# Optimization experiments

Measured on AMD Instinct MI355X. Metric: run time of the kernel, lower is better.

## Reference

```python
import jax, jax.numpy as jnp
import numpy as np

N, E = 20000, 320000
D, C = 128, 32          # node_dim, edge_dim
H, QK, V = 12, 32, 32   # heads, query_key_dim, value_dim
QP, VP = 8, 8           # query/value points
EPS_LN = 1e-5


def _lin_init(key, fan_in, fan_out):
    return jax.random.normal(key, (fan_in, fan_out), dtype=jnp.float32) / np.sqrt(fan_in)


def setup_inputs():
    key = jax.random.key(0)
    ks = jax.random.split(key, 24)
    inp = {}
    inp['R'] = jax.random.normal(ks[0], (N, 3, 3), dtype=jnp.float32)
    inp['t'] = jax.random.normal(ks[1], (N, 3), dtype=jnp.float32)
    inp['x'] = jax.random.normal(ks[2], (N, D), dtype=jnp.float32)
    inp['z'] = jax.random.normal(ks[3], (E, C), dtype=jnp.float32)
    inp['edge_index'] = jax.random.randint(ks[4], (2, E), 0, N, dtype=jnp.int64)
    inp['Wq'] = _lin_init(ks[5], D, QK * H)
    inp['Wk'] = _lin_init(ks[6], D, QK * H)
    inp['Wv'] = _lin_init(ks[7], D, V * H)
    inp['Wpair'] = _lin_init(ks[8], C, H)
    inp['spatial_coef'] = jnp.full((1, H), np.log(np.exp(1.0) - 1.0), dtype=jnp.float32)
    inp['Wqp'] = _lin_init(ks[9], D, QP * H * 3)
    inp['Wkp'] = _lin_init(ks[10], D, QP * H * 3)
    inp['Wvp'] = _lin_init(ks[11], D, VP * H * 3)
    d_out_in = H * C + H * V + H * VP * 7  # 384 + 384 + 672 = 1440
    inp['Wo'] = _lin_init(ks[12], d_out_in, D)
    inp['bo'] = jnp.zeros((D,), dtype=jnp.float32)
    inp['ln1_g'] = jnp.ones((D,), dtype=jnp.float32)
    inp['ln1_b'] = jnp.zeros((D,), dtype=jnp.float32)
    inp['mlp_w1'] = _lin_init(ks[13], D, D)
    inp['mlp_b1'] = jnp.zeros((D,), dtype=jnp.float32)
    inp['mlp_w2'] = _lin_init(ks[14], D, D)
    inp['mlp_b2'] = jnp.zeros((D,), dtype=jnp.float32)
    inp['mlp_w3'] = _lin_init(ks[15], D, D)
    inp['mlp_b3'] = jnp.zeros((D,), dtype=jnp.float32)
    inp['ln2_g'] = jnp.ones((D,), dtype=jnp.float32)
    inp['ln2_b'] = jnp.zeros((D,), dtype=jnp.float32)
    return inp


def _scatter_softmax(logits, seg, n):
    # numerically stable per-destination-node softmax over incoming edges
    m = jax.ops.segment_max(logits, seg, num_segments=n)
    m = jnp.where(jnp.isfinite(m), m, 0.0)
    e = jnp.exp(logits - m[seg])
    s = jax.ops.segment_sum(e, seg, num_segments=n)
    return e / s[seg]


def _ln(h, g, b):
    mu = jnp.mean(h, axis=-1, keepdims=True)
    var = jnp.var(h, axis=-1, keepdims=True)
    return (h - mu) / jnp.sqrt(var + EPS_LN) * g + b


def _local_to_global(R, t, p):  # p: (N, P, 3) -> R p + t
    return jnp.einsum('nij,npj->npi', R, p) + t[:, None, :]


def _global_to_local(R, t, q):  # q: (N, P, 3) -> R^T (q - t)
    return jnp.einsum('nji,npj->npi', R, q - t[:, None, :])


def reference(R, t, x, z, edge_index, Wq, Wk, Wv, Wpair, spatial_coef, Wqp, Wkp, Wvp,
              Wo, bo, ln1_g, ln1_b, mlp_w1, mlp_b1, mlp_w2, mlp_b2, mlp_w3, mlp_b3,
              ln2_g, ln2_b):
    n = x.shape[0]
    src, dst = edge_index[0], edge_index[1]

    # --- node logits ---
    q = (x @ Wq).reshape(n, H, QK)
    k = (x @ Wk).reshape(n, H, QK)
    logits_node = jnp.sum(q[src] * k[dst], axis=-1) / np.sqrt(QK)  # (E, H)

    # --- pair logits ---
    logits_pair = z @ Wpair  # (E, H)

    # --- spatial logits ---
    qp = _local_to_global(R, t, (x @ Wqp).reshape(n, H * QP, 3)).reshape(n, H, QP * 3)
    kp = _local_to_global(R, t, (x @ Wkp).reshape(n, H * QP, 3)).reshape(n, H, QP * 3)
    sum_sq_dist = jnp.sum((qp[src] - kp[dst]) ** 2, axis=-1)  # (E, H)
    gamma = jax.nn.softplus(spatial_coef)  # (1, H)
    logits_spatial = sum_sq_dist * (-gamma * np.sqrt(2.0 / (9.0 * QP)) / 2.0)

    logits = (logits_node + logits_pair + logits_spatial) * np.sqrt(1.0 / 3.0)
    alpha = _scatter_softmax(logits, src, n)  # (E, H)

    # --- pair aggregation: (E,H,1)*(E,1,C) scatter-sum -> (N, H*C) ---
    feat_p2n = jax.ops.segment_sum(alpha[:, :, None] * z[:, None, :], src, num_segments=n).reshape(n, -1)

    # --- node aggregation ---
    v = (x @ Wv).reshape(n, H, V)
    feat_node = jax.ops.segment_sum(alpha[:, :, None] * v[dst], src, num_segments=n).reshape(n, -1)

    # --- spatial aggregation ---
    vp = _local_to_global(R, t, (x @ Wvp).reshape(n, H * VP, 3)).reshape(n, H, VP, 3)
    aggr = jax.ops.segment_sum(alpha[:, :, None, None] * vp[dst], src, num_segments=n)  # (N,H,VP,3)
    loc = _global_to_local(R, t, aggr.reshape(n, H * VP, 3))  # (N, H*VP, 3)
    nrm = jnp.linalg.norm(loc, axis=-1)
    dirn = loc / jnp.maximum(nrm[..., None], 1e-8)
    feat_spatial = jnp.concatenate([loc.reshape(n, -1), nrm.reshape(n, -1), dirn.reshape(n, -1)], axis=-1)

    feat_all = jnp.concatenate([feat_p2n, feat_node, feat_spatial], axis=-1) @ Wo + bo
    h = _ln(x + feat_all, ln1_g, ln1_b)
    m = jax.nn.relu(h @ mlp_w1 + mlp_b1)
    m = jax.nn.relu(m @ mlp_w2 + mlp_b2) @ mlp_w3 + mlp_b3
    return _ln(h + m, ln2_g, ln2_b)
```

## Files before the change

### kernel.cpp

```cpp
#include <hip/hip_runtime.h>
#include <hip/hip_bf16.h>
#include <math.h>

#define NN 20000
#define EE 320000
#define PQ_COLS  384
#define PQP_COLS 288
#define PKP_COLS 288
#define QE_COLS  768
#define VE_COLS  672
#define KE_COLS  768
#define FCOLS 1440

typedef __attribute__((ext_vector_type(8))) short bf16x8v;
typedef __attribute__((ext_vector_type(4))) float f32x4v;

__device__ __forceinline__ float b2f(unsigned short u) {
  return __uint_as_float(((unsigned)u) << 16);
}
__device__ __forceinline__ unsigned short f2bu(float f) {
  __hip_bfloat16 h = __float2bfloat16(f);
  return *reinterpret_cast<unsigned short*>(&h);
}

__global__ void cvt_x(const float* __restrict__ x, __hip_bfloat16* __restrict__ XB)
{
  int i = (blockIdx.x*256 + threadIdx.x) * 4;
  if (i >= NN*128) return;
  float4 v = *(const float4*)&x[i];
  XB[i+0] = __float2bfloat16(v.x); XB[i+1] = __float2bfloat16(v.y);
  XB[i+2] = __float2bfloat16(v.z); XB[i+3] = __float2bfloat16(v.w);
}

__global__ void cvt_w(const float* __restrict__ Wq, const float* __restrict__ Wk,
                      const float* __restrict__ Wv, const float* __restrict__ Wqp,
                      const float* __restrict__ Wkp, const float* __restrict__ Wvp,
                      const float* __restrict__ Wo,
                      __hip_bfloat16* __restrict__ WBt, __hip_bfloat16* __restrict__ WoT)
{
  int idx = blockIdx.x*256 + threadIdx.x;
  if (idx < 2016*128) {
    int c = idx >> 7, k = idx & 127;
    float v;
    if      (c < 384)  v = Wq [k*384 + c];
    else if (c < 768)  v = Wk [k*384 + (c-384)];
    else if (c < 1152) v = Wv [k*384 + (c-768)];
    else if (c < 1440) v = Wqp[k*288 + (c-1152)];
    else if (c < 1728) v = Wkp[k*288 + (c-1440)];
    else               v = Wvp[k*288 + (c-1728)];
    WBt[idx] = __float2bfloat16(v);
  } else {
    int j = idx - 2016*128;
    if (j < 128*1440) {
      int c = j / 1440, k = j - c*1440;
      WoT[j] = __float2bfloat16(Wo[k*128 + c]);
    }
  }
}

__global__ __launch_bounds__(256) void proj_mfma(
    const __hip_bfloat16* __restrict__ XB, const __hip_bfloat16* __restrict__ WBt,
    float* __restrict__ Pq, float* __restrict__ Pqp, float* __restrict__ Pkp,
    __hip_bfloat16* __restrict__ KE, __hip_bfloat16* __restrict__ VE)
{
  __shared__ short A_lds[64*136];
  __shared__ short B_lds[128*136];
  const int t = threadIdx.x;
  const int n0 = blockIdx.x * 64;
  const int c0 = blockIdx.y * 128;
  {
    int r = t >> 2, kc = (t & 3) * 32;
    int gr = n0 + r; if (gr >= NN) gr = NN-1;
    const uint4* src = (const uint4*)(XB + (size_t)gr*128 + kc);
    uint4 v0 = src[0], v1 = src[1], v2 = src[2], v3 = src[3];
    *(uint4*)&A_lds[r*136 + kc +  0] = v0;
    *(uint4*)&A_lds[r*136 + kc +  8] = v1;
    *(uint4*)&A_lds[r*136 + kc + 16] = v2;
    *(uint4*)&A_lds[r*136 + kc + 24] = v3;
  }
  {
    int cI = t >> 1, ko = (t & 1) * 64;
    int gc = c0 + cI; if (gc > 2015) gc = 2015;
    const uint4* src = (const uint4*)(WBt + (size_t)gc*128 + ko);
    #pragma unroll
    for (int j = 0; j < 8; j++)
      *(uint4*)&B_lds[cI*136 + ko + j*8] = src[j];
  }
  __syncthreads();
  const int lane = t & 63, wid = t >> 6;
  const int wm = wid >> 1, wn = wid & 1;
  const int lrow = lane >> 4, lcol = lane & 15;
  f32x4v zero = {0.f, 0.f, 0.f, 0.f};
  f32x4v acc[2][4];
  #pragma unroll
  for (int i = 0; i < 2; i++)
    #pragma unroll
    for (int j = 0; j < 4; j++) acc[i][j] = zero;
  #pragma unroll
  for (int ks = 0; ks < 4; ks++) {
    int kb = ks*32 + lrow*8;
    bf16x8v a0 = *(const bf16x8v*)&A_lds[(wm*32 +      lcol)*136 + kb];
    bf16x8v a1 = *(const bf16x8v*)&A_lds[(wm*32 + 16 + lcol)*136 + kb];
    #pragma unroll
    for (int nt = 0; nt < 4; nt++) {
      bf16x8v b = *(const bf16x8v*)&B_lds[(wn*64 + nt*16 + lcol)*136 + kb];
      acc[0][nt] = __builtin_amdgcn_mfma_f32_16x16x32_bf16(a0, b, acc[0][nt], 0, 0, 0);
      acc[1][nt] = __builtin_amdgcn_mfma_f32_16x16x32_bf16(a1, b, acc[1][nt], 0, 0, 0);
    }
  }
  #pragma unroll
  for (int nt = 0; nt < 4; nt++) {
    int colb = c0 + wn*64 + nt*16;
    if (colb >= 2016) continue;
    int col = colb + lcol;
    #pragma unroll
    for (int mt = 0; mt < 2; mt++) {
      #pragma unroll
      for (int r = 0; r < 4; r++) {
        int grow = n0 + wm*32 + mt*16 + lrow*4 + r;
        if (grow >= NN) continue;
        float v = acc[mt][nt][r];
        if      (col < 384)  Pq[(size_t)grow*PQ_COLS + col] = v;
        else if (col < 768)  { int d = col-384; KE[(size_t)grow*KE_COLS + (d>>5)*64 + (d&31)] = __float2bfloat16(v); }
        else if (col < 1152) VE[(size_t)grow*VE_COLS + (col-768)] = __float2bfloat16(v);
        else if (col < 1440) Pqp[(size_t)grow*PQP_COLS + (col-1152)] = v;
        else if (col < 1728) Pkp[(size_t)grow*PKP_COLS + (col-1440)] = v;
        else                 VE[(size_t)grow*VE_COLS + 384 + (col-1728)] = __float2bfloat16(v);
      }
    }
  }
}

__global__ __launch_bounds__(256) void prep_node(
    const float* __restrict__ Pq, const float* __restrict__ Pqp, const float* __restrict__ Pkp,
    const float* __restrict__ R, const float* __restrict__ tr, const float* __restrict__ spc,
    __hip_bfloat16* __restrict__ QE, __hip_bfloat16* __restrict__ KE,
    __hip_bfloat16* __restrict__ VE)
{
  __shared__ float qpg[288];
  __shared__ float skk[12], cf[12];
  const int n = blockIdx.x, t = threadIdx.x;
  if (t < 12) { cf[t] = log1pf(expf(spc[t])) * (1.f/12.f); skk[t] = 0.f; }
  __syncthreads();
  const float* Rn = R + (size_t)n*9;
  const float r0=Rn[0],r1=Rn[1],r2=Rn[2],r3=Rn[3],r4=Rn[4],r5=Rn[5],r6=Rn[6],r7=Rn[7],r8=Rn[8];
  const float t0=tr[n*3],t1=tr[n*3+1],t2=tr[n*3+2];
  for (int task = t; task < 288; task += 256) {
    if (task < 96) {
      const float* p = Pqp + (size_t)n*PQP_COLS + task*3;
      float l0=p[0],l1=p[1],l2=p[2];
      qpg[task*3+0] = r0*l0+r1*l1+r2*l2+t0;
      qpg[task*3+1] = r3*l0+r4*l1+r5*l2+t1;
      qpg[task*3+2] = r6*l0+r7*l1+r8*l2+t2;
    } else if (task < 192) {
      int j = task-96, h = j>>3, jj = j&7;
      const float* p = Pkp + (size_t)n*PKP_COLS + h*24 + jj*3;
      float l0=p[0],l1=p[1],l2=p[2];
      __hip_bfloat16 b0=__float2bfloat16(r0*l0+r1*l1+r2*l2+t0);
      __hip_bfloat16 b1=__float2bfloat16(r3*l0+r4*l1+r5*l2+t1);
      __hip_bfloat16 b2=__float2bfloat16(r6*l0+r7*l1+r8*l2+t2);
      __hip_bfloat16* o = KE + (size_t)n*KE_COLS + h*64 + 32 + jj*3;
      o[0]=b0; o[1]=b1; o[2]=b2;
      float f0=__bfloat162float(b0), f1=__bfloat162float(b1), f2=__bfloat162float(b2);
      atomicAdd(&skk[h], f0*f0 + f1*f1 + f2*f2);
    } else {
      __hip_bfloat16* p = VE + (size_t)n*VE_COLS + 384 + (task-192)*3;
      float l0=__bfloat162float(p[0]), l1=__bfloat162float(p[1]), l2=__bfloat162float(p[2]);
      p[0] = __float2bfloat16(r0*l0+r1*l1+r2*l2+t0);
      p[1] = __float2bfloat16(r3*l0+r4*l1+r5*l2+t1);
      p[2] = __float2bfloat16(r6*l0+r7*l1+r8*l2+t2);
    }
  }
  __syncthreads();
  #pragma unroll
  for (int u = 0; u < 3; u++) {
    int s = t + 256*u;
    int h = s >> 6, i = s & 63;
    float val = 0.f;
    if (i < 32)      val = 0.1020620726f * Pq[(size_t)n*PQ_COLS + h*32 + i];
    else if (i < 56) val = 1.15470053838f * cf[h] * qpg[h*24 + (i-32)];
    else if (i == 58 || i == 59) val = 1.0f;
    QE[(size_t)n*QE_COLS + s] = __float2bfloat16(val);
  }
  if (t < 96) {
    int h = t >> 3, i = t & 7;
    float skkp = -0.57735026919f * cf[h] * skk[h];
    __hip_bfloat16 hi = __float2bfloat16(skkp);
    float res = skkp - __bfloat162float(hi);
    __hip_bfloat16 outv;
    if (i == 2)      outv = hi;
    else if (i == 3) outv = __float2bfloat16(res);
    else             outv = __float2bfloat16(0.0f);
    KE[(size_t)n*KE_COLS + h*64 + 56 + i] = outv;
  }
}

__global__ __launch_bounds__(256) void pl_kernel(
    const float* __restrict__ z, const float* __restrict__ Wpair, float* __restrict__ PL)
{
  __shared__ float wp[384];
  const int t = threadIdx.x;
  for (int i = t; i < 384; i += 256) wp[i] = Wpair[i] * 0.57735026919f;
  __syncthreads();
  int e0 = blockIdx.x * 64;
  #pragma unroll
  for (int u = 0; u < 3; u++) {
    int idx = t + 256*u;
    int q = idx / 12, h = idx - 12*q;
    int e = e0 + q;
    if (q < 64 && e < EE) {
      const float* zr = z + (size_t)e*32;
      float s = 0.f;
      #pragma unroll
      for (int c = 0; c < 32; c++) s += zr[c] * wp[c*12 + h];
      PL[(size_t)e*12 + h] = s;
    }
  }
}

__global__ void count_edges(const int* __restrict__ ei, int* __restrict__ cnt)
{
  int e = blockIdx.x*256 + threadIdx.x;
  if (e < EE) atomicAdd(&cnt[ei[e]], 1);
}

__global__ __launch_bounds__(1024) void scan_csr(const int* __restrict__ cnt,
                                                 int* __restrict__ rowptr,
                                                 int* __restrict__ cursor)
{
  __shared__ int part[1024];
  int t = threadIdx.x;
  int base = t*20;
  int loc[20];
  int s = 0;
  #pragma unroll
  for (int i = 0; i < 20; i++) {
    int idx = base + i;
    int cc = (idx < NN) ? cnt[idx] : 0;
    loc[i] = s; s += cc;
  }
  part[t] = s;
  __syncthreads();
  for (int off = 1; off < 1024; off <<= 1) {
    int v = (t >= off) ? part[t-off] : 0;
    __syncthreads();
    part[t] += v;
    __syncthreads();
  }
  int pre = (t == 0) ? 0 : part[t-1];
  #pragma unroll
  for (int i = 0; i < 20; i++) {
    int idx = base + i;
    if (idx < NN) { rowptr[idx] = pre + loc[i]; cursor[idx] = pre + loc[i]; }
  }
  if (t == 1023) rowptr[NN] = part[1023];
}

__global__ void fill_csr(const int* __restrict__ ei, int* __restrict__ cursor,
                         int* __restrict__ eidx, int* __restrict__ dstE)
{
  int e = blockIdx.x*256 + threadIdx.x;
  if (e >= EE) return;
  int pos = atomicAdd(&cursor[ei[e]], 1);
  eidx[pos] = e;
  dstE[pos] = ei[EE + e];
}

__device__ __forceinline__ float dot8(const float* qr, uint4 v) {
  float s;
  s  = qr[0]*b2f((unsigned short)(v.x & 0xffffu));
  s += qr[1]*b2f((unsigned short)(v.x >> 16));
  s += qr[2]*b2f((unsigned short)(v.y & 0xffffu));
  s += qr[3]*b2f((unsigned short)(v.y >> 16));
  s += qr[4]*b2f((unsigned short)(v.z & 0xffffu));
  s += qr[5]*b2f((unsigned short)(v.z >> 16));
  s += qr[6]*b2f((unsigned short)(v.w & 0xffffu));
  s += qr[7]*b2f((unsigned short)(v.w >> 16));
  return s;
}

__global__ __launch_bounds__(256) void attn_wave(
    const __hip_bfloat16* __restrict__ QE,
    const __hip_bfloat16* __restrict__ KE,
    const __hip_bfloat16* __restrict__ VE,
    const float* __restrict__ z, const float* __restrict__ PL,
    const int* __restrict__ rowptr, const int* __restrict__ eidx,
    const int* __restrict__ dstE,
    const float* __restrict__ R, const float* __restrict__ tr,
    __hip_bfloat16* __restrict__ featB)
{
  __shared__ float sAgg[4][288];
  const int wid = threadIdx.x >> 6, lane = threadIdx.x & 63;
  const int n = blockIdx.x*4 + wid;

  float q0[8], q1[8];
  {
    const uint4* qrow = (const uint4*)(QE + (size_t)n*QE_COLS);
    uint4 Q0 = qrow[lane];
    q0[0]=b2f((unsigned short)(Q0.x&0xffffu)); q0[1]=b2f((unsigned short)(Q0.x>>16));
    q0[2]=b2f((unsigned short)(Q0.y&0xffffu)); q0[3]=b2f((unsigned short)(Q0.y>>16));
    q0[4]=b2f((unsigned short)(Q0.z&0xffffu)); q0[5]=b2f((unsigned short)(Q0.z>>16));
    q0[6]=b2f((unsigned short)(Q0.w&0xffffu)); q0[7]=b2f((unsigned short)(Q0.w>>16));
    if (lane < 32) {
      uint4 Q1 = qrow[64 + lane];
      q1[0]=b2f((unsigned short)(Q1.x&0xffffu)); q1[1]=b2f((unsigned short)(Q1.x>>16));
      q1[2]=b2f((unsigned short)(Q1.y&0xffffu)); q1[3]=b2f((unsigned short)(Q1.y>>16));
      q1[4]=b2f((unsigned short)(Q1.z&0xffffu)); q1[5]=b2f((unsigned short)(Q1.z>>16));
      q1[6]=b2f((unsigned short)(Q1.w&0xffffu)); q1[7]=b2f((unsigned short)(Q1.w>>16));
    } else {
      #pragma unroll
      for (int j = 0; j < 8; j++) q1[j] = 0.f;
    }
  }

  const int myh0 = (lane < 48) ? (lane >> 2) : ((8*lane - 384) / 24);
  const int myh1 = (128 + 8*lane) / 24;

  float mreg = -1e30f, sreg = 0.f;
  float accV0[8] = {}, accV1[8] = {}, accZ[12] = {};

  const int beg = rowptr[n], end = rowptr[n+1];
  for (int c0 = beg; c0 < end; c0 += 64) {
    const int cn = min(64, end - c0);
    int eL = (lane < cn) ? eidx[c0 + lane] : 0;
    int dL = (lane < cn) ? dstE[c0 + lane] : 0;
    for (int j = 0; j < cn; j++) {
      const int e   = __shfl(eL, j);
      const int dst = __shfl(dL, j);
      const uint4* ke = (const uint4*)(KE + (size_t)dst*KE_COLS);
      uint4 K0 = ke[lane];
      uint4 K1 = make_uint4(0,0,0,0);
      if (lane < 32) K1 = ke[64 + lane];
      const uint4* ve = (const uint4*)(VE + (size_t)dst*VE_COLS);
      uint4 V0 = ve[lane];
      uint4 V1 = make_uint4(0,0,0,0);
      if (lane < 20) V1 = ve[64 + lane];
      float zc = (lane < 32) ? z[(size_t)e*32 + lane] : 0.f;
      float pl = (lane < 12) ? PL[(size_t)e*12 + lane] : 0.f;
      float p0 = dot8(q0, K0);
      p0 += __shfl_xor(p0, 1); p0 += __shfl_xor(p0, 2); p0 += __shfl_xor(p0, 4);
      float p1 = dot8(q1, K1);
      p1 += __shfl_xor(p1, 1); p1 += __shfl_xor(p1, 2); p1 += __shfl_xor(p1, 4);
      float pa = __shfl(p0, (lane & 7) * 8);
      float pb = __shfl(p1, (lane & 3) * 8);
      float lg = ((lane < 8) ? pa : pb) + pl;
      float mn = fmaxf(mreg, lg);
      unsigned long long chg = __ballot(mn > mreg) & 0xFFFull;
      float w = expf(lg - mn);
      float r = expf(mreg - mn);
      mreg = mn;
      sreg = sreg * r + w;
      if (chg) {
        float rv0 = __shfl(r, myh0);
        #pragma unroll
        for (int q2 = 0; q2 < 8; q2++) accV0[q2] *= rv0;
        float rv1 = __shfl(r, myh1);
        if (lane < 20) {
          #pragma unroll
          for (int q2 = 0; q2 < 8; q2++) accV1[q2] *= rv1;
        }
        #pragma unroll
        for (int h = 0; h < 12; h++) accZ[h] *= __shfl(r, h);
      }
      float wv0 = __shfl(w, myh0);
      accV0[0] += wv0 * b2f((unsigned short)(V0.x & 0xffffu));
      accV0[1] += wv0 * b2f((unsigned short)(V0.x >> 16));
      accV0[2] += wv0 * b2f((unsigned short)(V0.y & 0xffffu));
      accV0[3] += wv0 * b2f((unsigned short)(V0.y >> 16));
      accV0[4] += wv0 * b2f((unsigned short)(V0.z & 0xffffu));
      accV0[5] += wv0 * b2f((unsigned short)(V0.z >> 16));
      accV0[6] += wv0 * b2f((unsigned short)(V0.w & 0xffffu));
      accV0[7] += wv0 * b2f((unsigned short)(V0.w >> 16));
      float wv1 = __shfl(w, myh1);
      if (lane < 20) {
        accV1[0] += wv1 * b2f((unsigned short)(V1.x & 0xffffu));
        accV1[1] += wv1 * b2f((unsigned short)(V1.x >> 16));
        accV1[2] += wv1 * b2f((unsigned short)(V1.y & 0xffffu));
        accV1[3] += wv1 * b2f((unsigned short)(V1.y >> 16));
        accV1[4] += wv1 * b2f((unsigned short)(V1.z & 0xffffu));
        accV1[5] += wv1 * b2f((unsigned short)(V1.z >> 16));
        accV1[6] += wv1 * b2f((unsigned short)(V1.w & 0xffffu));
        accV1[7] += wv1 * b2f((unsigned short)(V1.w >> 16));
      }
      #pragma unroll
      for (int h = 0; h < 12; h++) accZ[h] += __shfl(w, h) * zc;
    }
  }

  float inv = 0.f;
  if (lane < 12) inv = (sreg > 0.f) ? 1.f/sreg : 0.f;
  __hip_bfloat16* fr = featB + (size_t)n*FCOLS;
  #pragma unroll
  for (int h = 0; h < 12; h++) {
    float iv = __shfl(inv, h);
    if (lane < 32) fr[h*32 + lane] = __float2bfloat16(accZ[h] * iv);
  }
  float iv0 = __shfl(inv, myh0);
  if (lane < 48) {
    uint4 P;
    P.x = (unsigned)f2bu(accV0[0]*iv0) | ((unsigned)f2bu(accV0[1]*iv0) << 16);
    P.y = (unsigned)f2bu(accV0[2]*iv0) | ((unsigned)f2bu(accV0[3]*iv0) << 16);
    P.z = (unsigned)f2bu(accV0[4]*iv0) | ((unsigned)f2bu(accV0[5]*iv0) << 16);
    P.w = (unsigned)f2bu(accV0[6]*iv0) | ((unsigned)f2bu(accV0[7]*iv0) << 16);
    *(uint4*)(fr + 384 + lane*8) = P;
  } else {
    #pragma unroll
    for (int j2 = 0; j2 < 8; j2++) sAgg[wid][(lane-48)*8 + j2] = accV0[j2]*iv0;
  }
  float iv1 = __shfl(inv, myh1);
  if (lane < 20) {
    #pragma unroll
    for (int j2 = 0; j2 < 8; j2++) sAgg[wid][128 + lane*8 + j2] = accV1[j2]*iv1;
  }
  __syncthreads();
  {
    const float* Rn = R + (size_t)n*9;
    float t0 = tr[n*3], t1 = tr[n*3+1], t2 = tr[n*3+2];
    #pragma unroll
    for (int pp = 0; pp < 2; pp++) {
      int pt = lane + pp*64;
      if (pt < 96) {
        float d0 = sAgg[wid][pt*3+0] - t0;
        float d1 = sAgg[wid][pt*3+1] - t1;
        float d2 = sAgg[wid][pt*3+2] - t2;
        float l0 = Rn[0]*d0 + Rn[3]*d1 + Rn[6]*d2;
        float l1 = Rn[1]*d0 + Rn[4]*d1 + Rn[7]*d2;
        float l2 = Rn[2]*d0 + Rn[5]*d1 + Rn[8]*d2;
        float nr = sqrtf(l0*l0 + l1*l1 + l2*l2);
        float ivn = 1.f / fmaxf(nr, 1e-8f);
        fr[768 + pt*3+0] = __float2bfloat16(l0);
        fr[768 + pt*3+1] = __float2bfloat16(l1);
        fr[768 + pt*3+2] = __float2bfloat16(l2);
        fr[1056 + pt]    = __float2bfloat16(nr);
        fr[1152 + pt*3+0] = __float2bfloat16(l0*ivn);
        fr[1152 + pt*3+1] = __float2bfloat16(l1*ivn);
        fr[1152 + pt*3+2] = __float2bfloat16(l2*ivn);
      }
    }
  }
}

__global__ __launch_bounds__(256) void wo_mfma(
    const __hip_bfloat16* __restrict__ featB, const __hip_bfloat16* __restrict__ WoT,
    const float* __restrict__ bo, const float* __restrict__ x,
    float* __restrict__ xo, float* __restrict__ XO2)
{
  __shared__ short A_lds[64*104];
  __shared__ short B_lds[128*104];
  const int t = threadIdx.x;
  const int n0 = blockIdx.x * 64;
  const int ysl = blockIdx.y;
  const int kbeg = ysl ? 768 : 0;
  const int kend = ysl ? 1440 : 768;
  const int lane = t & 63, wid = t >> 6;
  const int wm = wid >> 1, wn = wid & 1;
  const int lrow = lane >> 4, lcol = lane & 15;
  f32x4v zero = {0.f, 0.f, 0.f, 0.f};
  f32x4v acc[2][4];
  #pragma unroll
  for (int i = 0; i < 2; i++)
    #pragma unroll
    for (int j = 0; j < 4; j++) acc[i][j] = zero;
  for (int k0 = kbeg; k0 < kend; k0 += 96) {
    __syncthreads();
    {
      int r = t >> 2, kc = (t & 3) * 24;
      int gr = n0 + r; if (gr >= NN) gr = NN-1;
      const uint4* src = (const uint4*)(featB + (size_t)gr*FCOLS + k0 + kc);
      uint4 v0 = src[0], v1 = src[1], v2 = src[2];
      *(uint4*)&A_lds[r*104 + kc +  0] = v0;
      *(uint4*)&A_lds[r*104 + kc +  8] = v1;
      *(uint4*)&A_lds[r*104 + kc + 16] = v2;
    }
    {
      int cI = t >> 1, ko = (t & 1) * 48;
      const uint4* src = (const uint4*)(WoT + (size_t)cI*1440 + k0 + ko);
      #pragma unroll
      for (int j = 0; j < 6; j++)
        *(uint4*)&B_lds[cI*104 + ko + j*8] = src[j];
    }
    __syncthreads();
    #pragma unroll
    for (int ks = 0; ks < 3; ks++) {
      int kb = ks*32 + lrow*8;
      bf16x8v a0 = *(const bf16x8v*)&A_lds[(wm*32 +      lcol)*104 + kb];
      bf16x8v a1 = *(const bf16x8v*)&A_lds[(wm*32 + 16 + lcol)*104 + kb];
      #pragma unroll
      for (int nt = 0; nt < 4; nt++) {
        bf16x8v b = *(const bf16x8v*)&B_lds[(wn*64 + nt*16 + lcol)*104 + kb];
        acc[0][nt] = __builtin_amdgcn_mfma_f32_16x16x32_bf16(a0, b, acc[0][nt], 0, 0, 0);
        acc[1][nt] = __builtin_amdgcn_mfma_f32_16x16x32_bf16(a1, b, acc[1][nt], 0, 0, 0);
      }
    }
  }
  #pragma unroll
  for (int nt = 0; nt < 4; nt++) {
    int col = wn*64 + nt*16 + lcol;
    float bv = bo[col];
    #pragma unroll
    for (int mt = 0; mt < 2; mt++) {
      #pragma unroll
      for (int r = 0; r < 4; r++) {
        int grow = n0 + wm*32 + mt*16 + lrow*4 + r;
        if (grow < NN) {
          if (ysl == 0)
            xo[(size_t)grow*128 + col] = acc[mt][nt][r] + bv + x[(size_t)grow*128 + col];
          else
            XO2[(size_t)grow*128 + col] = acc[mt][nt][r];
        }
      }
    }
  }
}

__global__ __launch_bounds__(256) void lnmlp2(
    const float* __restrict__ xo, const float* __restrict__ XO2,
    const float* __restrict__ g1, const float* __restrict__ b1v,
    const float* __restrict__ w1, const float* __restrict__ bb1,
    const float* __restrict__ w2, const float* __restrict__ bb2,
    const float* __restrict__ w3, const float* __restrict__ bb3,
    const float* __restrict__ g2, const float* __restrict__ b2v,
    float* __restrict__ out)
{
  __shared__ float smem[17344];
  float* hs   = smem;
  float* AT   = smem + 4224;
  float* bA   = smem + 8832;
  float* bB   = smem + 13056;
  float* mu_s = smem + 17280;
  float* rs_s = smem + 17312;

  const int t = threadIdx.x, n0 = blockIdx.x * 32;
  const int tx = t & 31, ty = t >> 5;
  const int c = t & 127, rhalf = t >> 7;
  const int w = t >> 6, lane = t & 63;

  for (int e = t; e < 4096; e += 256) {
    int r = e >> 7, cc = e & 127;
    hs[r*132 + cc] = xo[(size_t)(n0 + r)*128 + cc] + XO2[(size_t)(n0 + r)*128 + cc];
  }
  __syncthreads();
  for (int q = 0; q < 8; q++) {
    int r = w*8 + q;
    float v0 = hs[r*132 + lane], v1 = hs[r*132 + lane + 64];
    float s = v0 + v1, ss = v0*v0 + v1*v1;
    #pragma unroll
    for (int m2 = 32; m2 >= 1; m2 >>= 1) { s += __shfl_xor(s, m2); ss += __shfl_xor(ss, m2); }
    if (lane == 0) { float mu = s*(1.f/128.f); mu_s[r] = mu; rs_s[r] = rsqrtf(ss*(1.f/128.f) - mu*mu + 1e-5f); }
  }
  __syncthreads();
  for (int r = rhalf; r < 32; r += 2)
    hs[r*132 + c] = (hs[r*132 + c] - mu_s[r]) * rs_s[r] * g1[c] + b1v[c];
  __syncthreads();

#define MLP_LAYER(INB, OUTB, WG, BG, DO_RELU, DO_RES)                          \
  {                                                                            \
    for (int e = t; e < 4096; e += 256) {                                      \
      int kk = e >> 5, r = e & 31;                                             \
      AT[kk*36 + r] = INB[r*132 + kk];                                         \
    }                                                                          \
    __syncthreads();                                                           \
    float acc[4][4] = {};                                                      \
    const float4* Wg4 = (const float4*)(WG);                                   \
    for (int kk = 0; kk < 128; kk++) {                                         \
      float4 a4 = *(const float4*)&AT[kk*36 + ty*4];                           \
      float4 b4 = Wg4[kk*32 + tx];                                             \
      float av[4] = {a4.x, a4.y, a4.z, a4.w};                                  \
      float bv[4] = {b4.x, b4.y, b4.z, b4.w};                                  \
      _Pragma("unroll")                                                        \
      for (int i2 = 0; i2 < 4; i2++)                                           \
        _Pragma("unroll")                                                      \
        for (int j2 = 0; j2 < 4; j2++)                                         \
          acc[i2][j2] += av[i2] * bv[j2];                                      \
    }                                                                          \
    _Pragma("unroll")                                                          \
    for (int i2 = 0; i2 < 4; i2++) {                                           \
      int r = ty*4 + i2;                                                       \
      _Pragma("unroll")                                                        \
      for (int j2 = 0; j2 < 4; j2++) {                                         \
        int cc2 = tx*4 + j2;                                                   \
        float v = acc[i2][j2] + BG[cc2];                                       \
        if (DO_RES) v += hs[r*132 + cc2];                                      \
        OUTB[r*132 + cc2] = DO_RELU ? fmaxf(v, 0.f) : v;                       \
      }                                                                        \
    }                                                                          \
    __syncthreads();                                                           \
  }

  MLP_LAYER(hs, bA, w1, bb1, 1, 0)
  MLP_LAYER(bA, bB, w2, bb2, 1, 0)
  MLP_LAYER(bB, bA, w3, bb3, 0, 1)
#undef MLP_LAYER

  for (int q = 0; q < 8; q++) {
    int r = w*8 + q;
    float v0 = bA[r*132 + lane], v1 = bA[r*132 + lane + 64];
    float s = v0 + v1, ss = v0*v0 + v1*v1;
    #pragma unroll
    for (int m2 = 32; m2 >= 1; m2 >>= 1) { s += __shfl_xor(s, m2); ss += __shfl_xor(ss, m2); }
    if (lane == 0) { float mu = s*(1.f/128.f); mu_s[r] = mu; rs_s[r] = rsqrtf(ss*(1.f/128.f) - mu*mu + 1e-5f); }
  }
  __syncthreads();
  for (int r = rhalf; r < 32; r += 2)
    out[(size_t)(n0 + r)*128 + c] = (bA[r*132 + c] - mu_s[r]) * rs_s[r] * g2[c] + b2v[c];
}

__global__ void diag_ws(float* out, float v)
{
  if (blockIdx.x == 0 && threadIdx.x == 0) out[0] = v;
}

static inline size_t alup(size_t v) { return (v + 255) & ~(size_t)255; }

extern "C" void kernel_launch(void* const* d_in, const int* in_sizes, int n_in,
                              void* d_out, int out_size, void* d_ws, size_t ws_size,
                              hipStream_t stream)
{
  const float* R     = (const float*)d_in[0];
  const float* tr    = (const float*)d_in[1];
  const float* x     = (const float*)d_in[2];
  const float* z     = (const float*)d_in[3];
  const int*   ei    = (const int*)  d_in[4];
  const float* Wq    = (const float*)d_in[5];
  const float* Wk    = (const float*)d_in[6];
  const float* Wv    = (const float*)d_in[7];
  const float* Wpair = (const float*)d_in[8];
  const float* spc   = (const float*)d_in[9];
  const float* Wqp   = (const float*)d_in[10];
  const float* Wkp   = (const float*)d_in[11];
  const float* Wvp   = (const float*)d_in[12];
  const float* Wo    = (const float*)d_in[13];
  const float* bo    = (const float*)d_in[14];
  const float* g1    = (const float*)d_in[15];
  const float* b1v   = (const float*)d_in[16];
  const float* w1    = (const float*)d_in[17];
  const float* bb1   = (const float*)d_in[18];
  const float* w2    = (const float*)d_in[19];
  const float* bb2   = (const float*)d_in[20];
  const float* w3    = (const float*)d_in[21];
  const float* bb3   = (const float*)d_in[22];
  const float* g2    = (const float*)d_in[23];
  const float* b2v   = (const float*)d_in[24];
  float* out = (float*)d_out;
  char* ws = (char*)d_ws;

  size_t pq_b  = alup((size_t)NN*PQ_COLS*4);
  size_t pqp_b = alup((size_t)NN*PQP_COLS*4);
  size_t pkp_b = alup((size_t)NN*PKP_COLS*4);
  size_t region = pq_b + pqp_b + pkp_b;
  size_t fb_b = alup((size_t)NN*FCOLS*2);
  size_t pl_b = alup((size_t)EE*12*4);
  size_t xo2_b = alup((size_t)NN*128*4);
  size_t scr = (pl_b > xo2_b) ? pl_b : xo2_b;
  if (fb_b + scr > region) region = fb_b + scr;

  float* Pq  = (float*)ws;
  float* Pqp = (float*)(ws + pq_b);
  float* Pkp = (float*)(ws + pq_b + pqp_b);
  __hip_bfloat16* featB = (__hip_bfloat16*)ws;
  float* PL  = (float*)(ws + fb_b);
  float* XO2 = (float*)(ws + fb_b);

  size_t off = region;
  __hip_bfloat16* QE = (__hip_bfloat16*)(ws + off); off += alup((size_t)NN*QE_COLS*2);
  __hip_bfloat16* VE = (__hip_bfloat16*)(ws + off); off += alup((size_t)NN*VE_COLS*2);
  __hip_bfloat16* KE = (__hip_bfloat16*)(ws + off); off += alup((size_t)NN*KE_COLS*2);
  int* cnt = (int*)(ws + off);       off += alup((size_t)NN*4);
  int* rowptr = (int*)(ws + off);    off += alup((size_t)(NN+1)*4);
  int* cursor = (int*)(ws + off);    off += alup((size_t)NN*4);
  int* eidx = (int*)(ws + off);      off += alup((size_t)EE*4);
  int* dstE = (int*)(ws + off);      off += alup((size_t)EE*4);
  __hip_bfloat16* XB  = (__hip_bfloat16*)(ws + off); off += alup((size_t)NN*128*2);
  __hip_bfloat16* WBt = (__hip_bfloat16*)(ws + off); off += alup((size_t)2016*128*2);
  __hip_bfloat16* WoT = (__hip_bfloat16*)(ws + off); off += alup((size_t)128*1440*2);
  float* xo = out;

  if (ws_size < off) {
    diag_ws<<<1, 64, 0, stream>>>(out, (float)((double)ws_size / (1024.0*1024.0)));
    return;
  }

  hipMemsetAsync(cnt, 0, (size_t)NN*4, stream);

  cvt_x<<<(NN*128/4 + 255)/256, 256, 0, stream>>>(x, XB);
  cvt_w<<<(2016*128 + 128*1440 + 255)/256, 256, 0, stream>>>(Wq, Wk, Wv, Wqp, Wkp, Wvp, Wo, WBt, WoT);
  proj_mfma<<<dim3((NN + 63)/64, 16), 256, 0, stream>>>(XB, WBt, Pq, Pqp, Pkp, KE, VE);
  prep_node<<<NN, 256, 0, stream>>>(Pq, Pqp, Pkp, R, tr, spc, QE, KE, VE);
  pl_kernel<<<(EE + 63)/64, 256, 0, stream>>>(z, Wpair, PL);
  count_edges<<<EE/256, 256, 0, stream>>>(ei, cnt);
  scan_csr<<<1, 1024, 0, stream>>>(cnt, rowptr, cursor);
  fill_csr<<<EE/256, 256, 0, stream>>>(ei, cursor, eidx, dstE);
  attn_wave<<<NN/4, 256, 0, stream>>>(QE, KE, VE, z, PL, rowptr, eidx, dstE, R, tr, featB);
  wo_mfma<<<dim3((NN + 63)/64, 2), 256, 0, stream>>>(featB, WoT, bo, x, xo, XO2);
  lnmlp2<<<NN/32, 256, 0, stream>>>(xo, XO2, g1, b1v, w1, bb1, w2, bb2,
                                    w3, bb3, g2, b2v, out);
}
```

Before: 452.9 us.

## Fuse Wo projection with LayerNorm and MLP using bf16 MFMA layers

Merges the output projection and the LN/MLP/LN kernel into one kernel per 64-row tile. The full K loop over 1440 now runs in one block instead of a K-split across two blocks, and the tile stays in LDS. The three MLP layers switch from fp32 FMA to bf16 MFMA, with the weights pre-transposed to bf16 in cvt_w. This removes the xo/XO2 global round trips and one launch, but halves the grid parallelism of the Wo GEMM, reads B fragments for the MLP straight from global memory, and lowers MLP precision to bf16.

```diff
diff --git a/kernel.cpp b/kernel.cpp
--- a/kernel.cpp
+++ b/kernel.cpp
@@ -36,7 +36,11 @@
                       const float* __restrict__ Wv, const float* __restrict__ Wqp,
                       const float* __restrict__ Wkp, const float* __restrict__ Wvp,
                       const float* __restrict__ Wo,
-                      __hip_bfloat16* __restrict__ WBt, __hip_bfloat16* __restrict__ WoT)
+                      const float* __restrict__ w1, const float* __restrict__ w2,
+                      const float* __restrict__ w3,
+                      __hip_bfloat16* __restrict__ WBt, __hip_bfloat16* __restrict__ WoT,
+                      __hip_bfloat16* __restrict__ W1T, __hip_bfloat16* __restrict__ W2T,
+                      __hip_bfloat16* __restrict__ W3T)
 {
   int idx = blockIdx.x*256 + threadIdx.x;
   if (idx < 2016*128) {
@@ -49,12 +53,21 @@
     else if (c < 1728) v = Wkp[k*288 + (c-1440)];
     else               v = Wvp[k*288 + (c-1728)];
     WBt[idx] = __float2bfloat16(v);
-  } else {
-    int j = idx - 2016*128;
-    if (j < 128*1440) {
-      int c = j / 1440, k = j - c*1440;
-      WoT[j] = __float2bfloat16(Wo[k*128 + c]);
-    }
+    return;
+  }
+  int j = idx - 2016*128;
+  if (j < 128*1440) {
+    int c = j / 1440, k = j - c*1440;
+    WoT[j] = __float2bfloat16(Wo[k*128 + c]);
+    return;
+  }
+  int m = j - 128*1440;
+  if (m < 3*16384) {
+    int layer = m >> 14, cm = m & 16383;
+    int c = cm >> 7, k = cm & 127;
+    const float* w = (layer == 0) ? w1 : (layer == 1) ? w2 : w3;
+    __hip_bfloat16* o = (layer == 0) ? W1T : (layer == 1) ? W2T : W3T;
+    o[cm] = __float2bfloat16(w[k*128 + c]);
   }
 }
 
@@ -440,28 +453,37 @@
   }
 }
 
-__global__ __launch_bounds__(256) void wo_mfma(
+__global__ __launch_bounds__(256) void wo_mlp(
     const __hip_bfloat16* __restrict__ featB, const __hip_bfloat16* __restrict__ WoT,
     const float* __restrict__ bo, const float* __restrict__ x,
-    float* __restrict__ xo, float* __restrict__ XO2)
-{
-  __shared__ short A_lds[64*104];
-  __shared__ short B_lds[128*104];
+    const __hip_bfloat16* __restrict__ W1T, const float* __restrict__ bb1,
+    const __hip_bfloat16* __restrict__ W2T, const float* __restrict__ bb2,
+    const __hip_bfloat16* __restrict__ W3T, const float* __restrict__ bb3,
+    const float* __restrict__ g1, const float* __restrict__ b1v,
+    const float* __restrict__ g2, const float* __restrict__ b2v,
+    float* __restrict__ out)
+{
+  __shared__ float4 arenaV[3200];
+  __shared__ float mu_s[64], rs_s[64];
+  char* arena  = (char*)arenaV;
+  short* A_lds = (short*)arena;
+  short* B_lds = (short*)(arena + 13312);
+  float* hs    = (float*)arena;
+  short* actB  = (short*)(arena + 33792);
+
   const int t = threadIdx.x;
   const int n0 = blockIdx.x * 64;
-  const int ysl = blockIdx.y;
-  const int kbeg = ysl ? 768 : 0;
-  const int kend = ysl ? 1440 : 768;
   const int lane = t & 63, wid = t >> 6;
   const int wm = wid >> 1, wn = wid & 1;
   const int lrow = lane >> 4, lcol = lane & 15;
   f32x4v zero = {0.f, 0.f, 0.f, 0.f};
+
   f32x4v acc[2][4];
   #pragma unroll
   for (int i = 0; i < 2; i++)
     #pragma unroll
     for (int j = 0; j < 4; j++) acc[i][j] = zero;
-  for (int k0 = kbeg; k0 < kend; k0 += 96) {
+  for (int k0 = 0; k0 < 1440; k0 += 96) {
     __syncthreads();
     {
       int r = t >> 2, kc = (t & 3) * 24;
@@ -493,6 +515,7 @@
       }
     }
   }
+  __syncthreads();
   #pragma unroll
   for (int nt = 0; nt < 4; nt++) {
     int col = wn*64 + nt*16 + lcol;
@@ -501,47 +524,15 @@
     for (int mt = 0; mt < 2; mt++) {
       #pragma unroll
       for (int r = 0; r < 4; r++) {
-        int grow = n0 + wm*32 + mt*16 + lrow*4 + r;
-        if (grow < NN) {
-          if (ysl == 0)
-            xo[(size_t)grow*128 + col] = acc[mt][nt][r] + bv + x[(size_t)grow*128 + col];
-          else
-            XO2[(size_t)grow*128 + col] = acc[mt][nt][r];
-        }
+        int row = wm*32 + mt*16 + lrow*4 + r;
+        int gr = n0 + row; if (gr >= NN) gr = NN-1;
+        hs[row*132 + col] = acc[mt][nt][r] + bv + x[(size_t)gr*128 + col];
       }
     }
   }
-}
-
-__global__ __launch_bounds__(256) void lnmlp2(
-    const float* __restrict__ xo, const float* __restrict__ XO2,
-    const float* __restrict__ g1, const float* __restrict__ b1v,
-    const float* __restrict__ w1, const float* __restrict__ bb1,
-    const float* __restrict__ w2, const float* __restrict__ bb2,
-    const float* __restrict__ w3, const float* __restrict__ bb3,
-    const float* __restrict__ g2, const float* __restrict__ b2v,
-    float* __restrict__ out)
-{
-  __shared__ float smem[17344];
-  float* hs   = smem;
-  float* AT   = smem + 4224;
-  float* bA   = smem + 8832;
-  float* bB   = smem + 13056;
-  float* mu_s = smem + 17280;
-  float* rs_s = smem + 17312;
-
-  const int t = threadIdx.x, n0 = blockIdx.x * 32;
-  const int tx = t & 31, ty = t >> 5;
-  const int c = t & 127, rhalf = t >> 7;
-  const int w = t >> 6, lane = t & 63;
-
-  for (int e = t; e < 4096; e += 256) {
-    int r = e >> 7, cc = e & 127;
-    hs[r*132 + cc] = xo[(size_t)(n0 + r)*128 + cc] + XO2[(size_t)(n0 + r)*128 + cc];
-  }
-  __syncthreads();
-  for (int q = 0; q < 8; q++) {
-    int r = w*8 + q;
+  __syncthreads();
+  for (int q = 0; q < 16; q++) {
+    int r = wid*16 + q;
     float v0 = hs[r*132 + lane], v1 = hs[r*132 + lane + 64];
     float s = v0 + v1, ss = v0*v0 + v1*v1;
     #pragma unroll
@@ -549,60 +540,73 @@
     if (lane == 0) { float mu = s*(1.f/128.f); mu_s[r] = mu; rs_s[r] = rsqrtf(ss*(1.f/128.f) - mu*mu + 1e-5f); }
   }
   __syncthreads();
-  for (int r = rhalf; r < 32; r += 2)
-    hs[r*132 + c] = (hs[r*132 + c] - mu_s[r]) * rs_s[r] * g1[c] + b1v[c];
-  __syncthreads();
-
-#define MLP_LAYER(INB, OUTB, WG, BG, DO_RELU, DO_RES)                          \
-  {                                                                            \
-    for (int e = t; e < 4096; e += 256) {                                      \
-      int kk = e >> 5, r = e & 31;                                             \
-      AT[kk*36 + r] = INB[r*132 + kk];                                         \
-    }                                                                          \
-    __syncthreads();                                                           \
-    float acc[4][4] = {};                                                      \
-    const float4* Wg4 = (const float4*)(WG);                                   \
-    for (int kk = 0; kk < 128; kk++) {                                         \
-      float4 a4 = *(const float4*)&AT[kk*36 + ty*4];                           \
-      float4 b4 = Wg4[kk*32 + tx];                                             \
-      float av[4] = {a4.x, a4.y, a4.z, a4.w};                                  \
-      float bv[4] = {b4.x, b4.y, b4.z, b4.w};                                  \
-      _Pragma("unroll")                                                        \
-      for (int i2 = 0; i2 < 4; i2++)                                           \
-        _Pragma("unroll")                                                      \
-        for (int j2 = 0; j2 < 4; j2++)                                         \
-          acc[i2][j2] += av[i2] * bv[j2];                                      \
-    }                                                                          \
-    _Pragma("unroll")                                                          \
-    for (int i2 = 0; i2 < 4; i2++) {                                           \
-      int r = ty*4 + i2;                                                       \
-      _Pragma("unroll")                                                        \
-      for (int j2 = 0; j2 < 4; j2++) {                                         \
-        int cc2 = tx*4 + j2;                                                   \
-        float v = acc[i2][j2] + BG[cc2];                                       \
-        if (DO_RES) v += hs[r*132 + cc2];                                      \
-        OUTB[r*132 + cc2] = DO_RELU ? fmaxf(v, 0.f) : v;                       \
-      }                                                                        \
-    }                                                                          \
-    __syncthreads();                                                           \
-  }
-
-  MLP_LAYER(hs, bA, w1, bb1, 1, 0)
-  MLP_LAYER(bA, bB, w2, bb2, 1, 0)
-  MLP_LAYER(bB, bA, w3, bb3, 0, 1)
-#undef MLP_LAYER
-
-  for (int q = 0; q < 8; q++) {
-    int r = w*8 + q;
-    float v0 = bA[r*132 + lane], v1 = bA[r*132 + lane + 64];
+  for (int e = t; e < 8192; e += 256) {
+    int r = e >> 7, c = e & 127;
+    float v = (hs[r*132 + c] - mu_s[r]) * rs_s[r] * g1[c] + b1v[c];
+    hs[r*132 + c] = v;
+    actB[r*136 + c] = (short)f2bu(v);
+  }
+  __syncthreads();
+
+#define MLP_MFMA_LAYER(WT, BIAS, IS_LAST)                                       \
+  {                                                                             \
+    f32x4v acc2[2][4];                                                          \
+    _Pragma("unroll")                                                           \
+    for (int i = 0; i < 2; i++)                                                 \
+      _Pragma("unroll")                                                         \
+      for (int j = 0; j < 4; j++) acc2[i][j] = zero;                            \
+    _Pragma("unroll")                                                           \
+    for (int ks = 0; ks < 4; ks++) {                                            \
+      int kb = ks*32 + lrow*8;                                                  \
+      bf16x8v a0 = *(const bf16x8v*)&actB[(wm*32 +      lcol)*136 + kb];        \
+      bf16x8v a1 = *(const bf16x8v*)&actB[(wm*32 + 16 + lcol)*136 + kb];        \
+      _Pragma("unroll")                                                         \
+      for (int nt = 0; nt < 4; nt++) {                                          \
+        int col = wn*64 + nt*16 + lcol;                                         \
+        bf16x8v b = *(const bf16x8v*)(WT + (size_t)col*128 + kb);               \
+        acc2[0][nt] = __builtin_amdgcn_mfma_f32_16x16x32_bf16(a0, b, acc2[0][nt], 0, 0, 0); \
+        acc2[1][nt] = __builtin_amdgcn_mfma_f32_16x16x32_bf16(a1, b, acc2[1][nt], 0, 0, 0); \
+      }                                                                         \
+    }                                                                           \
+    __syncthreads();                                                            \
+    _Pragma("unroll")                                                           \
+    for (int nt = 0; nt < 4; nt++) {                                            \
+      int col = wn*64 + nt*16 + lcol;                                           \
+      float bv = BIAS[col];                                                     \
+      _Pragma("unroll")                                                         \
+      for (int mt = 0; mt < 2; mt++) {                                          \
+        _Pragma("unroll")                                                       \
+        for (int r = 0; r < 4; r++) {                                           \
+          int row = wm*32 + mt*16 + lrow*4 + r;                                 \
+          float v = acc2[mt][nt][r] + bv;                                       \
+          if (IS_LAST) hs[row*132 + col] += v;                                  \
+          else         actB[row*136 + col] = (short)f2bu(fmaxf(v, 0.f));        \
+        }                                                                       \
+      }                                                                         \
+    }                                                                           \
+    __syncthreads();                                                            \
+  }
+
+  MLP_MFMA_LAYER(W1T, bb1, 0)
+  MLP_MFMA_LAYER(W2T, bb2, 0)
+  MLP_MFMA_LAYER(W3T, bb3, 1)
+#undef MLP_MFMA_LAYER
+
+  for (int q = 0; q < 16; q++) {
+    int r = wid*16 + q;
+    float v0 = hs[r*132 + lane], v1 = hs[r*132 + lane + 64];
     float s = v0 + v1, ss = v0*v0 + v1*v1;
     #pragma unroll
     for (int m2 = 32; m2 >= 1; m2 >>= 1) { s += __shfl_xor(s, m2); ss += __shfl_xor(ss, m2); }
     if (lane == 0) { float mu = s*(1.f/128.f); mu_s[r] = mu; rs_s[r] = rsqrtf(ss*(1.f/128.f) - mu*mu + 1e-5f); }
   }
   __syncthreads();
-  for (int r = rhalf; r < 32; r += 2)
-    out[(size_t)(n0 + r)*128 + c] = (bA[r*132 + c] - mu_s[r]) * rs_s[r] * g2[c] + b2v[c];
+  for (int e = t; e < 8192; e += 256) {
+    int r = e >> 7, c = e & 127;
+    int gr = n0 + r;
+    if (gr < NN)
+      out[(size_t)gr*128 + c] = (hs[r*132 + c] - mu_s[r]) * rs_s[r] * g2[c] + b2v[c];
+  }
 }
 
 __global__ void diag_ws(float* out, float v)
@@ -650,16 +654,13 @@
   size_t region = pq_b + pqp_b + pkp_b;
   size_t fb_b = alup((size_t)NN*FCOLS*2);
   size_t pl_b = alup((size_t)EE*12*4);
-  size_t xo2_b = alup((size_t)NN*128*4);
-  size_t scr = (pl_b > xo2_b) ? pl_b : xo2_b;
-  if (fb_b + scr > region) region = fb_b + scr;
+  if (fb_b + pl_b > region) region = fb_b + pl_b;
 
   float* Pq  = (float*)ws;
   float* Pqp = (float*)(ws + pq_b);
   float* Pkp = (float*)(ws + pq_b + pqp_b);
   __hip_bfloat16* featB = (__hip_bfloat16*)ws;
   float* PL  = (float*)(ws + fb_b);
-  float* XO2 = (float*)(ws + fb_b);
 
   size_t off = region;
   __hip_bfloat16* QE = (__hip_bfloat16*)(ws + off); off += alup((size_t)NN*QE_COLS*2);
@@ -673,7 +674,9 @@
   __hip_bfloat16* XB  = (__hip_bfloat16*)(ws + off); off += alup((size_t)NN*128*2);
   __hip_bfloat16* WBt = (__hip_bfloat16*)(ws + off); off += alup((size_t)2016*128*2);
   __hip_bfloat16* WoT = (__hip_bfloat16*)(ws + off); off += alup((size_t)128*1440*2);
-  float* xo = out;
+  __hip_bfloat16* W1T = (__hip_bfloat16*)(ws + off); off += alup((size_t)128*128*2);
+  __hip_bfloat16* W2T = (__hip_bfloat16*)(ws + off); off += alup((size_t)128*128*2);
+  __hip_bfloat16* W3T = (__hip_bfloat16*)(ws + off); off += alup((size_t)128*128*2);
 
   if (ws_size < off) {
     diag_ws<<<1, 64, 0, stream>>>(out, (float)((double)ws_size / (1024.0*1024.0)));
@@ -683,7 +686,8 @@
   hipMemsetAsync(cnt, 0, (size_t)NN*4, stream);
 
   cvt_x<<<(NN*128/4 + 255)/256, 256, 0, stream>>>(x, XB);
-  cvt_w<<<(2016*128 + 128*1440 + 255)/256, 256, 0, stream>>>(Wq, Wk, Wv, Wqp, Wkp, Wvp, Wo, WBt, WoT);
+  cvt_w<<<(2016*128 + 128*1440 + 3*16384 + 255)/256, 256, 0, stream>>>(
+      Wq, Wk, Wv, Wqp, Wkp, Wvp, Wo, w1, w2, w3, WBt, WoT, W1T, W2T, W3T);
   proj_mfma<<<dim3((NN + 63)/64, 16), 256, 0, stream>>>(XB, WBt, Pq, Pqp, Pkp, KE, VE);
   prep_node<<<NN, 256, 0, stream>>>(Pq, Pqp, Pkp, R, tr, spc, QE, KE, VE);
   pl_kernel<<<(EE + 63)/64, 256, 0, stream>>>(z, Wpair, PL);
@@ -691,7 +695,7 @@
   scan_csr<<<1, 1024, 0, stream>>>(cnt, rowptr, cursor);
   fill_csr<<<EE/256, 256, 0, stream>>>(ei, cursor, eidx, dstE);
   attn_wave<<<NN/4, 256, 0, stream>>>(QE, KE, VE, z, PL, rowptr, eidx, dstE, R, tr, featB);
-  wo_mfma<<<dim3((NN + 63)/64, 2), 256, 0, stream>>>(featB, WoT, bo, x, xo, XO2);
-  lnmlp2<<<NN/32, 256, 0, stream>>>(xo, XO2, g1, b1v, w1, bb1, w2, bb2,
-                                    w3, bb3, g2, b2v, out);
-}
+  wo_mlp<<<(NN + 63)/64, 256, 0, stream>>>(featB, WoT, bo, x,
+                                           W1T, bb1, W2T, bb2, W3T, bb3,
+                                           g1, b1v, g2, b2v, out);
+}
```

After: 409.0 us. 1.11x faster.
